# Kernel tuning notes

Measured on AMD Instinct MI355X. Metric: run time of the kernel, lower is better.

## Reference

```python
import jax, jax.numpy as jnp
import numpy as np

B, F0, D = 4096, 39, 16
CROSS_LAYER_SIZE = (128, 128)


def _he_uniform(key, shape):
    fan_in = int(np.prod(shape[:-1]))
    limit = np.sqrt(6.0 / fan_in)
    return jax.random.uniform(key, shape, jnp.float32, -limit, limit)


def setup_inputs() -> dict:
    key = jax.random.key(0)
    k_x, k_f0, k_f1, k_w, k_b = jax.random.split(key, 5)
    x = jax.random.normal(k_x, (B, F0, D), dtype=jnp.float32)
    # field_nums with direct=False: [39, 128//2=64, 64]
    f0 = _he_uniform(k_f0, (F0 * F0, CROSS_LAYER_SIZE[0]))          # (1521, 128)
    f1 = _he_uniform(k_f1, (F0 * (CROSS_LAYER_SIZE[0] // 2), CROSS_LAYER_SIZE[1]))  # (2496, 128)
    out_dim = CROSS_LAYER_SIZE[0] // 2 + CROSS_LAYER_SIZE[1]        # 192
    dense_w = _he_uniform(k_w, (out_dim, 1))
    dense_b = jnp.zeros((1,), dtype=jnp.float32)
    return {"x": x, "f0": f0, "f1": f1, "dense_w": dense_w, "dense_b": dense_b}


def reference(x, f0, f1, dense_w, dense_b):
    # CIN forward (direct=False, use_bias=False, use_residual=False, relu)
    # x: (B, F0, D)
    filters = [f0, f1]
    n_layers = len(CROSS_LAYER_SIZE)
    h = x  # hidden state, (B, Fk, D)
    finals = []
    for idx, L in enumerate(CROSS_LAYER_SIZE):
        Fk = h.shape[1]
        # filter f_ has shape (F0*Fk, L) with i (field of x0) major, j (field of h) minor
        Wr = filters[idx].reshape(F0, Fk, L)
        # fused outer product + conv1d (kernel width 1 == matmul over i,j):
        # z[b, m, d] = sum_{i,j} x[b,i,d] * h[b,j,d] * W[i,j,m]
        z = jnp.einsum('bid,bjd,ijm->bmd', x, h, Wr)  # (B, L, D)
        z = jax.nn.relu(z)
        if idx != n_layers - 1:
            # split along feature-map axis: first half feeds next layer,
            # second half goes to output
            h = z[:, : L // 2, :]
            finals.append(z[:, L // 2:, :])
        else:
            finals.append(z)
    result = jnp.sum(jnp.concatenate(finals, axis=1), axis=-1)  # (B, 192)
    return result @ dense_w + dense_b  # (B, 1)
```

## Files before the change

### kernel.cpp

```cpp
#include <hip/hip_runtime.h>


typedef _Float16 h2    __attribute__((ext_vector_type(2)));
typedef _Float16 f16x8 __attribute__((ext_vector_type(8)));
typedef __attribute__((ext_vector_type(16))) float f32x16;

#define XBB 1160
#define L0C 30
#define NCH 110

__device__ __constant__ int IG0[L0C] = {0,0,0,0,0, 1,1,1,1,1, 2,2,2,2, 3,3,3,3, 4,4,4, 5,5,5, 6,6, 7,7, 8, 9};
__device__ __constant__ int JG0[L0C] = {0,1,2,3,4, 0,1,2,3,4, 1,2,3,4, 1,2,3,4, 2,3,4, 2,3,4, 3,4, 3,4, 4, 4};
#define IG0T(c) ((c)<5?0:(c)<10?1:(c)<14?2:(c)<18?3:(c)<21?4:(c)<24?5:(c)<26?6:(c)<28?7:(c)<29?8:9)
#define JG0T(c) ((c)<10?((c)%5):(c)<18?(((c)-10)%4+1):(c)<24?(((c)-18)%3+2):(c)<28?(((c)-24)%2+3):4)

__global__ __launch_bounds__(256)
void CIN_repack(const float* __restrict__ f0, const float* __restrict__ f1,
                uint4* __restrict__ ws)
{
    const int tid  = blockIdx.x * 256 + threadIdx.x;
    const int n    = tid & 127;
    const int slot = tid >> 7;
    const int half = slot & 1;
    const int kh   = (slot >> 1) & 1;
    const int ch   = slot >> 2;
    float v[8];
    if (ch < L0C) {
        const int ig = IG0[ch], jg = JG0[ch];
        const int i = ig * 4 + kh * 2 + half;
#pragma unroll
        for (int t = 0; t < 8; ++t) {
            const int j = jg * 8 + t;
            float val = 0.f;
            if (i < 39 && j < 39 && j >= i) {
                val = f0[(i * 39 + j) * 128 + n];
                if (j > i) val += f0[(j * 39 + i) * 128 + n];
            }
            v[t] = val;
        }
    } else {
        const int c1 = ch - L0C;
        const int jg = c1 / 5, ig = c1 - jg * 5;
        const int j = jg * 4 + kh * 2 + half;
#pragma unroll
        for (int t = 0; t < 8; ++t) {
            const int i = ig * 8 + t;
            v[t] = (i < 39) ? f1[(i * 64 + j) * 128 + n] : 0.f;
        }
    }
    union { h2 h[4]; uint4 q; } pk;
#pragma unroll
    for (int t = 0; t < 4; ++t)
        pk.h[t] = h2{(_Float16)v[2 * t], (_Float16)v[2 * t + 1]};
    const int lane = half * 32 + (n & 31);
    const int cg   = n >> 5;
    ws[ch * 512 + kh * 256 + cg * 64 + lane] = pk.q;
}

__global__ __launch_bounds__(256, 2)
void CIN_main(const float* __restrict__ x,
              const char* __restrict__ wsB,
              const float* __restrict__ dw,
              const float* __restrict__ db,
              float* __restrict__ out)
{
    __shared__ __align__(16) _Float16 xsH[8 * XBB];
    __shared__ __align__(4)  _Float16 hsH[8][64][18];
    __shared__ float dws[192];
    __shared__ float red[4][4];

    const int tid  = threadIdx.x;
    const int w    = tid >> 6;
    const int wp   = w >> 1;
    const int wn   = w & 1;
    const int lane = tid & 63;
    const int half = lane >> 5;
    const int d    = lane & 15;
    const int bsel = (lane >> 4) & 1;
    const int col  = lane & 31;

    const char* wbase = wsB + lane * 16 + wn * 2048 + 2560;
    f16x8 Bb[2][2][2];
    auto loadBg = [&](int ch, f16x8 (&B)[2][2]) {
        const char* p0 = wbase + (size_t)ch * 8192;
        B[0][0] = *(const f16x8*)(p0 - 2560);
        B[0][1] = *(const f16x8*)(p0 - 1536);
        B[1][0] = *(const f16x8*)(p0 + 1536);
        B[1][1] = *(const f16x8*)(p0 + 2560);
    };

    loadBg(0, Bb[0]);
    loadBg(1, Bb[1]);

    const float4* xg4 = (const float4*)(x + (size_t)blockIdx.x * 8 * 624);
    for (int e4 = tid; e4 < 1248; e4 += 256) {
        float4 v = xg4[e4];
        int bb = e4 / 156, r = e4 - bb * 156;
        int i = r >> 2, d0 = (r & 3) * 4;
        _Float16* bp = xsH + bb * XBB + i;
        bp[(d0 + 0) * 72] = (_Float16)v.x; bp[(d0 + 1) * 72] = (_Float16)v.y;
        bp[(d0 + 2) * 72] = (_Float16)v.z; bp[(d0 + 3) * 72] = (_Float16)v.w;
    }
    if (tid < 128) { int bb = tid >> 4, dd = tid & 15; xsH[bb * XBB + dd * 72 + 39] = (_Float16)0.f; }
    if (tid < 192) dws[tid] = dw[tid];
    __syncthreads();

    const _Float16* xrow[2] = {
        xsH + ((wp * 2 + 0) * 2 + bsel) * XBB + d * 72,
        xsH + ((wp * 2 + 1) * 2 + bsel) * XBB + d * 72
    };

    h2 xw[2][20];
#pragma unroll
    for (int p = 0; p < 2; ++p)
#pragma unroll
        for (int w5 = 0; w5 < 5; ++w5) {
            union { f16x8 v; h2 h[4]; } u;
            u.v = *(const f16x8*)(xrow[p] + w5 * 8);
#pragma unroll
            for (int q = 0; q < 4; ++q) xw[p][w5 * 4 + q] = u.h[q];
        }

    f32x16 acc[2][2];
#pragma unroll
    for (int p = 0; p < 2; ++p)
#pragma unroll
        for (int nq = 0; nq < 2; ++nq)
#pragma unroll
            for (int r = 0; r < 16; ++r) acc[p][nq][r] = 0.f;

    h2 sp2[2][2];

#pragma unroll
    for (int c = 0; c < L0C; ++c) {
        const int ig = IG0T(c);
        const int jg = JG0T(c);
        if ((c == 0) || (IG0T(c) != IG0T(c - 1))) {
#pragma unroll
            for (int p = 0; p < 2; ++p)
#pragma unroll
                for (int kh = 0; kh < 2; ++kh) {
                    const h2 pr = xw[p][ig * 2 + kh];
                    const _Float16 vv = half ? pr.y : pr.x;
                    sp2[p][kh] = h2{vv, vv};
                }
        }
#pragma unroll
        for (int p = 0; p < 2; ++p) {
            union { h2 h[4]; f16x8 v; } a0, a1;
#pragma unroll
            for (int q = 0; q < 4; ++q) {
                a0.h[q] = sp2[p][0] * xw[p][jg * 4 + q];
                a1.h[q] = sp2[p][1] * xw[p][jg * 4 + q];
            }
            acc[p][0] = __builtin_amdgcn_mfma_f32_32x32x16_f16(a0.v, Bb[c & 1][0][0], acc[p][0], 0, 0, 0);
            acc[p][1] = __builtin_amdgcn_mfma_f32_32x32x16_f16(a0.v, Bb[c & 1][0][1], acc[p][1], 0, 0, 0);
            acc[p][0] = __builtin_amdgcn_mfma_f32_32x32x16_f16(a1.v, Bb[c & 1][1][0], acc[p][0], 0, 0, 0);
            acc[p][1] = __builtin_amdgcn_mfma_f32_32x32x16_f16(a1.v, Bb[c & 1][1][1], acc[p][1], 0, 0, 0);
        }
        loadBg(c + 2, Bb[c & 1]);
    }

    float cs[4] = {0.f, 0.f, 0.f, 0.f};
    if (wn == 0) {
#pragma unroll
        for (int p = 0; p < 2; ++p)
#pragma unroll
            for (int nq = 0; nq < 2; ++nq)
#pragma unroll
                for (int r = 0; r < 16; r += 2) {
                    const int row = (r & 3) + 8 * (r >> 2) + 4 * half;
                    h2 pr = h2{(_Float16)fmaxf(acc[p][nq][r],     0.f),
                               (_Float16)fmaxf(acc[p][nq][r + 1], 0.f)};
                    *(h2*)&hsH[(wp * 2 + p) * 2 + (row >> 4)][nq * 32 + col][row & 15] = pr;
                }
    } else {
#pragma unroll
        for (int nq = 0; nq < 2; ++nq) {
            const float dwv = dws[nq * 32 + col];
#pragma unroll
            for (int p = 0; p < 2; ++p)
#pragma unroll
                for (int r = 0; r < 16; ++r) {
                    const int row = (r & 3) + 8 * (r >> 2) + 4 * half;
                    cs[p * 2 + (row >> 4)] += fmaxf(acc[p][nq][r], 0.f) * dwv;
                }
        }
    }
#pragma unroll
    for (int p = 0; p < 2; ++p)
#pragma unroll
        for (int nq = 0; nq < 2; ++nq)
#pragma unroll
            for (int r = 0; r < 16; ++r) acc[p][nq][r] = 0.f;
    __syncthreads();

#pragma unroll 1
    for (int o2 = 0; o2 < 4; ++o2) {
#pragma unroll
        for (int u = 0; u < 20; ++u) {
            const int ig2 = u % 5;
            if (ig2 == 0) {
                const int jb = (o2 * 4 + u / 5) * 4;
#pragma unroll
                for (int p = 0; p < 2; ++p)
#pragma unroll
                    for (int kh = 0; kh < 2; ++kh) {
                        const _Float16 s = hsH[(wp * 2 + p) * 2 + bsel][jb + kh * 2 + half][d];
                        sp2[p][kh] = h2{s, s};
                    }
            }
#pragma unroll
            for (int p = 0; p < 2; ++p) {
                union { h2 h[4]; f16x8 v; } a0, a1;
#pragma unroll
                for (int q = 0; q < 4; ++q) {
                    a0.h[q] = sp2[p][0] * xw[p][ig2 * 4 + q];
                    a1.h[q] = sp2[p][1] * xw[p][ig2 * 4 + q];
                }
                acc[p][0] = __builtin_amdgcn_mfma_f32_32x32x16_f16(a0.v, Bb[u & 1][0][0], acc[p][0], 0, 0, 0);
                acc[p][1] = __builtin_amdgcn_mfma_f32_32x32x16_f16(a0.v, Bb[u & 1][0][1], acc[p][1], 0, 0, 0);
                acc[p][0] = __builtin_amdgcn_mfma_f32_32x32x16_f16(a1.v, Bb[u & 1][1][0], acc[p][0], 0, 0, 0);
                acc[p][1] = __builtin_amdgcn_mfma_f32_32x32x16_f16(a1.v, Bb[u & 1][1][1], acc[p][1], 0, 0, 0);
            }
            int chn = 30 + o2 * 20 + u + 2; if (chn > NCH - 1) chn = NCH - 1;
            loadBg(chn, Bb[u & 1]);
        }
    }

#pragma unroll
    for (int nq = 0; nq < 2; ++nq) {
        const float dwv = dws[64 + (wn * 2 + nq) * 32 + col];
#pragma unroll
        for (int p = 0; p < 2; ++p)
#pragma unroll
            for (int r = 0; r < 16; ++r) {
                const int row = (r & 3) + 8 * (r >> 2) + 4 * half;
                cs[p * 2 + (row >> 4)] += fmaxf(acc[p][nq][r], 0.f) * dwv;
            }
    }
#pragma unroll
    for (int rr = 0; rr < 4; ++rr)
#pragma unroll
        for (int off = 32; off > 0; off >>= 1)
            cs[rr] += __shfl_xor(cs[rr], off, 64);
    if (lane == 0) {
#pragma unroll
        for (int rr = 0; rr < 4; ++rr) red[w][rr] = cs[rr];
    }
    __syncthreads();
    if (tid < 8) {
        const int wpp = tid >> 2, l = tid & 3;
        out[blockIdx.x * 8 + tid] = red[wpp * 2][l] + red[wpp * 2 + 1][l] + db[0];
    }
}

extern "C" void kernel_launch(void* const* d_in, const int* in_sizes, int n_in,
                              void* d_out, int out_size, void* d_ws, size_t ws_size,
                              hipStream_t stream)
{
    const float* x  = (const float*)d_in[0];
    const float* f0 = (const float*)d_in[1];
    const float* f1 = (const float*)d_in[2];
    const float* dw = (const float*)d_in[3];
    const float* db = (const float*)d_in[4];
    float* out = (float*)d_out;

    CIN_repack<<<dim3(220), dim3(256), 0, stream>>>(f0, f1, (uint4*)d_ws);
    CIN_main<<<dim3(512), dim3(256), 0, stream>>>(x, (const char*)d_ws, dw, db, out);
}
```

Baseline: 121.0 us.

## Split per-wave batch pairs across 8 waves and rotate layer-1 weight order per block

Doubles the block to 512 threads so each wave handles one batch-pair instead of two, halving accumulator and x-register state per wave and raising the number of resident waves. It also rotates the starting weight-chunk group of the second layer by block index so concurrent blocks read different weight chunks, spreading L2/cache traffic. Each weight fragment is now loaded for half as many MFMAs, so weight-load traffic per block doubles.

```diff
diff --git a/kernel.cpp b/kernel.cpp
--- a/kernel.cpp
+++ b/kernel.cpp
@@ -57,7 +57,7 @@
     ws[ch * 512 + kh * 256 + cg * 64 + lane] = pk.q;
 }
 
-__global__ __launch_bounds__(256, 2)
+__global__ __launch_bounds__(512, 4)
 void CIN_main(const float* __restrict__ x,
               const char* __restrict__ wsB,
               const float* __restrict__ dw,
@@ -67,7 +67,7 @@
     __shared__ __align__(16) _Float16 xsH[8 * XBB];
     __shared__ __align__(4)  _Float16 hsH[8][64][18];
     __shared__ float dws[192];
-    __shared__ float red[4][4];
+    __shared__ float red[8][2];
 
     const int tid  = threadIdx.x;
     const int w    = tid >> 6;
@@ -78,6 +78,7 @@
     const int d    = lane & 15;
     const int bsel = (lane >> 4) & 1;
     const int col  = lane & 31;
+    const int rot  = blockIdx.x & 15;
 
     const char* wbase = wsB + lane * 16 + wn * 2048 + 2560;
     f16x8 Bb[2][2][2];
@@ -93,7 +94,7 @@
     loadBg(1, Bb[1]);
 
     const float4* xg4 = (const float4*)(x + (size_t)blockIdx.x * 8 * 624);
-    for (int e4 = tid; e4 < 1248; e4 += 256) {
+    for (int e4 = tid; e4 < 1248; e4 += 512) {
         float4 v = xg4[e4];
         int bb = e4 / 156, r = e4 - bb * 156;
         int i = r >> 2, d0 = (r & 3) * 4;
@@ -105,31 +106,23 @@
     if (tid < 192) dws[tid] = dw[tid];
     __syncthreads();
 
-    const _Float16* xrow[2] = {
-        xsH + ((wp * 2 + 0) * 2 + bsel) * XBB + d * 72,
-        xsH + ((wp * 2 + 1) * 2 + bsel) * XBB + d * 72
-    };
-
-    h2 xw[2][20];
-#pragma unroll
-    for (int p = 0; p < 2; ++p)
-#pragma unroll
-        for (int w5 = 0; w5 < 5; ++w5) {
-            union { f16x8 v; h2 h[4]; } u;
-            u.v = *(const f16x8*)(xrow[p] + w5 * 8);
-#pragma unroll
-            for (int q = 0; q < 4; ++q) xw[p][w5 * 4 + q] = u.h[q];
-        }
-
-    f32x16 acc[2][2];
-#pragma unroll
-    for (int p = 0; p < 2; ++p)
-#pragma unroll
-        for (int nq = 0; nq < 2; ++nq)
-#pragma unroll
-            for (int r = 0; r < 16; ++r) acc[p][nq][r] = 0.f;
-
-    h2 sp2[2][2];
+    const _Float16* xrow = xsH + (wp * 2 + bsel) * XBB + d * 72;
+    h2 xw[20];
+#pragma unroll
+    for (int w5 = 0; w5 < 5; ++w5) {
+        union { f16x8 v; h2 h[4]; } u;
+        u.v = *(const f16x8*)(xrow + w5 * 8);
+#pragma unroll
+        for (int q = 0; q < 4; ++q) xw[w5 * 4 + q] = u.h[q];
+    }
+
+    f32x16 acc[2];
+#pragma unroll
+    for (int nq = 0; nq < 2; ++nq)
+#pragma unroll
+        for (int r = 0; r < 16; ++r) acc[nq][r] = 0.f;
+
+    h2 sp2[2];
 
 #pragma unroll
     for (int c = 0; c < L0C; ++c) {
@@ -137,62 +130,52 @@
         const int jg = JG0T(c);
         if ((c == 0) || (IG0T(c) != IG0T(c - 1))) {
 #pragma unroll
-            for (int p = 0; p < 2; ++p)
-#pragma unroll
-                for (int kh = 0; kh < 2; ++kh) {
-                    const h2 pr = xw[p][ig * 2 + kh];
-                    const _Float16 vv = half ? pr.y : pr.x;
-                    sp2[p][kh] = h2{vv, vv};
-                }
-        }
-#pragma unroll
-        for (int p = 0; p < 2; ++p) {
-            union { h2 h[4]; f16x8 v; } a0, a1;
-#pragma unroll
-            for (int q = 0; q < 4; ++q) {
-                a0.h[q] = sp2[p][0] * xw[p][jg * 4 + q];
-                a1.h[q] = sp2[p][1] * xw[p][jg * 4 + q];
-            }
-            acc[p][0] = __builtin_amdgcn_mfma_f32_32x32x16_f16(a0.v, Bb[c & 1][0][0], acc[p][0], 0, 0, 0);
-            acc[p][1] = __builtin_amdgcn_mfma_f32_32x32x16_f16(a0.v, Bb[c & 1][0][1], acc[p][1], 0, 0, 0);
-            acc[p][0] = __builtin_amdgcn_mfma_f32_32x32x16_f16(a1.v, Bb[c & 1][1][0], acc[p][0], 0, 0, 0);
-            acc[p][1] = __builtin_amdgcn_mfma_f32_32x32x16_f16(a1.v, Bb[c & 1][1][1], acc[p][1], 0, 0, 0);
-        }
-        loadBg(c + 2, Bb[c & 1]);
-    }
-
-    float cs[4] = {0.f, 0.f, 0.f, 0.f};
+            for (int kh = 0; kh < 2; ++kh) {
+                const h2 pr = xw[ig * 2 + kh];
+                const _Float16 vv = half ? pr.y : pr.x;
+                sp2[kh] = h2{vv, vv};
+            }
+        }
+        union { h2 h[4]; f16x8 v; } a0, a1;
+#pragma unroll
+        for (int q = 0; q < 4; ++q) {
+            a0.h[q] = sp2[0] * xw[jg * 4 + q];
+            a1.h[q] = sp2[1] * xw[jg * 4 + q];
+        }
+        acc[0] = __builtin_amdgcn_mfma_f32_32x32x16_f16(a0.v, Bb[c & 1][0][0], acc[0], 0, 0, 0);
+        acc[1] = __builtin_amdgcn_mfma_f32_32x32x16_f16(a0.v, Bb[c & 1][0][1], acc[1], 0, 0, 0);
+        acc[0] = __builtin_amdgcn_mfma_f32_32x32x16_f16(a1.v, Bb[c & 1][1][0], acc[0], 0, 0, 0);
+        acc[1] = __builtin_amdgcn_mfma_f32_32x32x16_f16(a1.v, Bb[c & 1][1][1], acc[1], 0, 0, 0);
+        const int lc = (c < 28) ? (c + 2) : (30 + rot * 5 + (c - 28));
+        loadBg(lc, Bb[c & 1]);
+    }
+
+    float cs[2] = {0.f, 0.f};
     if (wn == 0) {
 #pragma unroll
-        for (int p = 0; p < 2; ++p)
-#pragma unroll
-            for (int nq = 0; nq < 2; ++nq)
-#pragma unroll
-                for (int r = 0; r < 16; r += 2) {
-                    const int row = (r & 3) + 8 * (r >> 2) + 4 * half;
-                    h2 pr = h2{(_Float16)fmaxf(acc[p][nq][r],     0.f),
-                               (_Float16)fmaxf(acc[p][nq][r + 1], 0.f)};
-                    *(h2*)&hsH[(wp * 2 + p) * 2 + (row >> 4)][nq * 32 + col][row & 15] = pr;
-                }
+        for (int nq = 0; nq < 2; ++nq)
+#pragma unroll
+            for (int r = 0; r < 16; r += 2) {
+                const int row = (r & 3) + 8 * (r >> 2) + 4 * half;
+                h2 pr = h2{(_Float16)fmaxf(acc[nq][r],     0.f),
+                           (_Float16)fmaxf(acc[nq][r + 1], 0.f)};
+                *(h2*)&hsH[wp * 2 + (row >> 4)][nq * 32 + col][row & 15] = pr;
+            }
     } else {
 #pragma unroll
         for (int nq = 0; nq < 2; ++nq) {
             const float dwv = dws[nq * 32 + col];
 #pragma unroll
-            for (int p = 0; p < 2; ++p)
-#pragma unroll
-                for (int r = 0; r < 16; ++r) {
-                    const int row = (r & 3) + 8 * (r >> 2) + 4 * half;
-                    cs[p * 2 + (row >> 4)] += fmaxf(acc[p][nq][r], 0.f) * dwv;
-                }
-        }
-    }
-#pragma unroll
-    for (int p = 0; p < 2; ++p)
-#pragma unroll
-        for (int nq = 0; nq < 2; ++nq)
-#pragma unroll
-            for (int r = 0; r < 16; ++r) acc[p][nq][r] = 0.f;
+            for (int r = 0; r < 16; ++r) {
+                const int row = (r & 3) + 8 * (r >> 2) + 4 * half;
+                cs[row >> 4] += fmaxf(acc[nq][r], 0.f) * dwv;
+            }
+        }
+    }
+#pragma unroll
+    for (int nq = 0; nq < 2; ++nq)
+#pragma unroll
+        for (int r = 0; r < 16; ++r) acc[nq][r] = 0.f;
     __syncthreads();
 
 #pragma unroll 1
@@ -200,30 +183,27 @@
 #pragma unroll
         for (int u = 0; u < 20; ++u) {
             const int ig2 = u % 5;
+            const int g   = (o2 * 4 + u / 5 + rot) & 15;
             if (ig2 == 0) {
-                const int jb = (o2 * 4 + u / 5) * 4;
-#pragma unroll
-                for (int p = 0; p < 2; ++p)
-#pragma unroll
-                    for (int kh = 0; kh < 2; ++kh) {
-                        const _Float16 s = hsH[(wp * 2 + p) * 2 + bsel][jb + kh * 2 + half][d];
-                        sp2[p][kh] = h2{s, s};
-                    }
-            }
-#pragma unroll
-            for (int p = 0; p < 2; ++p) {
-                union { h2 h[4]; f16x8 v; } a0, a1;
-#pragma unroll
-                for (int q = 0; q < 4; ++q) {
-                    a0.h[q] = sp2[p][0] * xw[p][ig2 * 4 + q];
-                    a1.h[q] = sp2[p][1] * xw[p][ig2 * 4 + q];
+                const int jb = g * 4;
+#pragma unroll
+                for (int kh = 0; kh < 2; ++kh) {
+                    const _Float16 s = hsH[wp * 2 + bsel][jb + kh * 2 + half][d];
+                    sp2[kh] = h2{s, s};
                 }
-                acc[p][0] = __builtin_amdgcn_mfma_f32_32x32x16_f16(a0.v, Bb[u & 1][0][0], acc[p][0], 0, 0, 0);
-                acc[p][1] = __builtin_amdgcn_mfma_f32_32x32x16_f16(a0.v, Bb[u & 1][0][1], acc[p][1], 0, 0, 0);
-                acc[p][0] = __builtin_amdgcn_mfma_f32_32x32x16_f16(a1.v, Bb[u & 1][1][0], acc[p][0], 0, 0, 0);
-                acc[p][1] = __builtin_amdgcn_mfma_f32_32x32x16_f16(a1.v, Bb[u & 1][1][1], acc[p][1], 0, 0, 0);
-            }
-            int chn = 30 + o2 * 20 + u + 2; if (chn > NCH - 1) chn = NCH - 1;
+            }
+            union { h2 h[4]; f16x8 v; } a0, a1;
+#pragma unroll
+            for (int q = 0; q < 4; ++q) {
+                a0.h[q] = sp2[0] * xw[ig2 * 4 + q];
+                a1.h[q] = sp2[1] * xw[ig2 * 4 + q];
+            }
+            acc[0] = __builtin_amdgcn_mfma_f32_32x32x16_f16(a0.v, Bb[u & 1][0][0], acc[0], 0, 0, 0);
+            acc[1] = __builtin_amdgcn_mfma_f32_32x32x16_f16(a0.v, Bb[u & 1][0][1], acc[1], 0, 0, 0);
+            acc[0] = __builtin_amdgcn_mfma_f32_32x32x16_f16(a1.v, Bb[u & 1][1][0], acc[0], 0, 0, 0);
+            acc[1] = __builtin_amdgcn_mfma_f32_32x32x16_f16(a1.v, Bb[u & 1][1][1], acc[1], 0, 0, 0);
+            const int g2  = (o2 * 4 + (u + 2) / 5 + rot) & 15;
+            const int chn = 30 + g2 * 5 + (u + 2) % 5;
             loadBg(chn, Bb[u & 1]);
         }
     }
@@ -232,25 +212,23 @@
     for (int nq = 0; nq < 2; ++nq) {
         const float dwv = dws[64 + (wn * 2 + nq) * 32 + col];
 #pragma unroll
-        for (int p = 0; p < 2; ++p)
-#pragma unroll
-            for (int r = 0; r < 16; ++r) {
-                const int row = (r & 3) + 8 * (r >> 2) + 4 * half;
-                cs[p * 2 + (row >> 4)] += fmaxf(acc[p][nq][r], 0.f) * dwv;
-            }
-    }
-#pragma unroll
-    for (int rr = 0; rr < 4; ++rr)
+        for (int r = 0; r < 16; ++r) {
+            const int row = (r & 3) + 8 * (r >> 2) + 4 * half;
+            cs[row >> 4] += fmaxf(acc[nq][r], 0.f) * dwv;
+        }
+    }
+#pragma unroll
+    for (int rr = 0; rr < 2; ++rr)
 #pragma unroll
         for (int off = 32; off > 0; off >>= 1)
             cs[rr] += __shfl_xor(cs[rr], off, 64);
     if (lane == 0) {
-#pragma unroll
-        for (int rr = 0; rr < 4; ++rr) red[w][rr] = cs[rr];
+        red[w][0] = cs[0];
+        red[w][1] = cs[1];
     }
     __syncthreads();
     if (tid < 8) {
-        const int wpp = tid >> 2, l = tid & 3;
+        const int wpp = tid >> 1, l = tid & 1;
         out[blockIdx.x * 8 + tid] = red[wpp * 2][l] + red[wpp * 2 + 1][l] + db[0];
     }
 }
@@ -267,5 +245,5 @@
     float* out = (float*)d_out;
 
     CIN_repack<<<dim3(220), dim3(256), 0, stream>>>(f0, f1, (uint4*)d_ws);
-    CIN_main<<<dim3(512), dim3(256), 0, stream>>>(x, (const char*)d_ws, dw, db, out);
+    CIN_main<<<dim3(512), dim3(512), 0, stream>>>(x, (const char*)d_ws, dw, db, out);
 }
```

New measurement: 132.8 us. +9.7%, slower.
